# Kernel optimization log

Measured on AMD Instinct MI355X. Metric: run time of the kernel, lower is better.

The kernel has to match this reference:

```python
import jax, jax.numpy as jnp
import numpy as np

NUM_POINTS = 16384
OVERSAMPLE = 3
IMPORTANCE_RATIO = 0.75


def point_sample(feat, coords):
    """grid_sample(bilinear, align_corners=False, zero padding) at [0,1]^2 coords.
    feat: (N, C, H, W); coords: (N, P, 2) with coords[...,0]=x (width), [...,1]=y.
    Returns (N, C, P)."""
    N, C, H, W = feat.shape
    # grid_sample with g = 2c-1, align_corners=False -> pixel = c*size - 0.5
    x = coords[..., 0] * W - 0.5
    y = coords[..., 1] * H - 0.5
    x0 = jnp.floor(x)
    y0 = jnp.floor(y)
    x1 = x0 + 1.0
    y1 = y0 + 1.0
    wx1 = x - x0
    wx0 = 1.0 - wx1
    wy1 = y - y0
    wy0 = 1.0 - wy1
    featf = feat.reshape(N, C, H * W)

    def gather(yi, xi):
        valid = (xi >= 0) & (xi <= W - 1) & (yi >= 0) & (yi <= H - 1)
        xic = jnp.clip(xi, 0, W - 1).astype(jnp.int32)
        yic = jnp.clip(yi, 0, H - 1).astype(jnp.int32)
        idx = yic * W + xic  # (N, P)
        v = jnp.take_along_axis(featf, idx[:, None, :], axis=2)  # (N, C, P)
        return v * valid[:, None, :].astype(feat.dtype)

    out = (gather(y0, x0) * (wy0 * wx0)[:, None, :]
           + gather(y0, x1) * (wy0 * wx1)[:, None, :]
           + gather(y1, x0) * (wy1 * wx0)[:, None, :]
           + gather(y1, x1) * (wy1 * wx1)[:, None, :])
    return out


def calculate_uncertainty(logits):
    """logits: (N, C, P) -> (N, P) uncertainty = top2 - top1 (<= 0)."""
    if logits.shape[1] == 1:
        return -jnp.abs(logits)[:, 0, :]
    top2 = jax.lax.top_k(jnp.moveaxis(logits, 1, -1), 2)[0]  # (N, P, 2)
    return top2[..., 1] - top2[..., 0]


def sample_point_coords(coarse_logits):
    """get_uncertain_point_coords_with_randomness (torch.no_grad branch)."""
    N = coarse_logits.shape[0]
    num_sampled = NUM_POINTS * OVERSAMPLE
    num_imp = int(IMPORTANCE_RATIO * NUM_POINTS)
    num_rand = NUM_POINTS - num_imp
    k1, k2 = jax.random.split(jax.random.key(7))
    cand = jax.random.uniform(k1, (N, num_sampled, 2), dtype=jnp.float32)
    cand_logits = point_sample(coarse_logits, cand)  # (N, C, S)
    unc = calculate_uncertainty(cand_logits)  # (N, S)
    idx = jax.lax.top_k(unc, num_imp)[1]  # (N, num_imp)
    imp = jnp.take_along_axis(cand, idx[..., None], axis=1)  # (N, num_imp, 2)
    rand = jax.random.uniform(k2, (N, num_rand, 2), dtype=jnp.float32)
    return jnp.concatenate([imp, rand], axis=1)  # (N, P, 2)


def point_head(fine, coarse_pts, w0, b0, w1, b1, w2, b2, wp, bp):
    x = jnp.concatenate([fine, coarse_pts], axis=1)  # (N, nin+C, P)
    for w, b in ((w0, b0), (w1, b1), (w2, b2)):
        x = jax.nn.relu(jnp.einsum('oc,ncp->nop', w, x) + b[None, :, None])
        x = jnp.concatenate([x, coarse_pts], axis=1)  # coarse_pred_each_layer
    return jnp.einsum('oc,ncp->nop', wp, x) + bp[None, :, None]  # (N, C, P)


def setup_inputs() -> dict:
    key = jax.random.key(0)
    ks = jax.random.split(key, 8)
    N, C, Hc, Wc = 8, 19, 64, 64
    nin, Hf, Wf = 256, 128, 128
    fin = nin + C  # 275
    return {
        'coarse_sem_seg_logits': jax.random.normal(ks[0], (N, C, Hc, Wc), jnp.float32),
        'features': jax.random.normal(ks[1], (N, nin, Hf, Wf), jnp.float32),
        'w0': jax.random.normal(ks[2], (nin, fin), jnp.float32) * (2.0 / fin) ** 0.5,
        'b0': jnp.zeros((nin,), jnp.float32),
        'w1': jax.random.normal(ks[3], (nin, fin), jnp.float32) * (2.0 / fin) ** 0.5,
        'b1': jnp.zeros((nin,), jnp.float32),
        'w2': jax.random.normal(ks[4], (nin, fin), jnp.float32) * (2.0 / fin) ** 0.5,
        'b2': jnp.zeros((nin,), jnp.float32),
        'wp': jax.random.normal(ks[5], (C, fin), jnp.float32) * 0.001,
        'bp': jnp.zeros((C,), jnp.float32),
    }


def reference(coarse_sem_seg_logits, features, w0, b0, w1, b1, w2, b2, wp, bp):
    # training-mode forward of PointRendSemSegHead
    point_coords = jax.lax.stop_gradient(
        sample_point_coords(jax.lax.stop_gradient(coarse_sem_seg_logits)))
    coarse_pts = point_sample(coarse_sem_seg_logits, point_coords)  # (N, C, P)
    fine_pts = point_sample(features, point_coords)  # (N, nin, P)
    point_logits = point_head(fine_pts, coarse_pts, w0, b0, w1, b1, w2, b2, wp, bp)
    return coarse_sem_seg_logits, point_logits, point_coords
```

## Files before the change

### kernel.cpp

```cpp
#include <hip/hip_runtime.h>
#include <stdint.h>

#pragma clang fp contract(off)

#define NB    8
#define CCH   19
#define CSTR  20
#define FCH   256
#define FIN   275
#define KP    288
#define NPTS  16384
#define NSAMP 49152
#define NIMP  12288
#define NRAND 4096
#define SORT_M 65536
#define CHUNK  8192
#define TP    64
#define XROW  640
#define WBF_OFF (4u << 20)
#define CTR_OFF (4718592u)
#define FTR_OFF (8u << 20)
#define FTR_BYTES (134217728ull / 2)

typedef __attribute__((ext_vector_type(8))) short bf16x8;
typedef __attribute__((ext_vector_type(4))) float f32x4;

__host__ __device__ __forceinline__ uint32_t rotl32(uint32_t v, int r) {
  return (v << r) | (v >> (32 - r));
}

__host__ __device__ __forceinline__ void tf2x32(uint32_t k0, uint32_t k1,
                                                uint32_t x0, uint32_t x1,
                                                uint32_t* o0, uint32_t* o1) {
  const uint32_t ks2 = k0 ^ k1 ^ 0x1BD11BDAu;
  x0 += k0; x1 += k1;
#define TF_R(r) { x0 += x1; x1 = rotl32(x1, (r)); x1 ^= x0; }
  TF_R(13) TF_R(15) TF_R(26) TF_R(6)
  x0 += k1;  x1 += ks2 + 1u;
  TF_R(17) TF_R(29) TF_R(16) TF_R(24)
  x0 += ks2; x1 += k0 + 2u;
  TF_R(13) TF_R(15) TF_R(26) TF_R(6)
  x0 += k0;  x1 += k1 + 3u;
  TF_R(17) TF_R(29) TF_R(16) TF_R(24)
  x0 += k1;  x1 += ks2 + 4u;
  TF_R(13) TF_R(15) TF_R(26) TF_R(6)
  x0 += ks2; x1 += k0 + 5u;
#undef TF_R
  *o0 = x0; *o1 = x1;
}

__device__ __forceinline__ float u01_at(uint32_t k0, uint32_t k1, uint32_t i) {
  uint32_t o0, o1;
  tf2x32(k0, k1, 0u, i, &o0, &o1);
  const uint32_t b = o0 ^ o1;
  const float f = __uint_as_float((b >> 9) | 0x3f800000u) - 1.0f;
  return fmaxf(0.0f, f);
}

__device__ __forceinline__ unsigned short f2bf(float f) {
  const uint32_t u = __float_as_uint(f);
  return (unsigned short)((u + 0x7fffu + ((u >> 16) & 1u)) >> 16);
}

__device__ __forceinline__ float bf2f(unsigned short h) {
  return __uint_as_float((uint32_t)h << 16);
}

template <int SZ>
__device__ __forceinline__ void interp(float cx, float cy, int* off, float* wgt) {
  const float X = cx * (float)SZ - 0.5f, Y = cy * (float)SZ - 0.5f;
  const float x0f = floorf(X), y0f = floorf(Y);
  const float fx = X - x0f, fy = Y - y0f;
  const float wx0 = 1.0f - fx, wy0 = 1.0f - fy;
  const int x0 = (int)x0f, y0 = (int)y0f;
  const int x0c = min(max(x0, 0), SZ - 1), x1c = min(max(x0 + 1, 0), SZ - 1);
  const int y0c = min(max(y0, 0), SZ - 1), y1c = min(max(y0 + 1, 0), SZ - 1);
  const bool vx0 = (x0 >= 0) & (x0 <= SZ - 1), vx1 = (x0 >= -1) & (x0 <= SZ - 2);
  const bool vy0 = (y0 >= 0) & (y0 <= SZ - 1), vy1 = (y0 >= -1) & (y0 <= SZ - 2);
  off[0] = y0c * SZ + x0c; wgt[0] = (vy0 & vx0) ? wy0 * wx0 : 0.0f;
  off[1] = y0c * SZ + x1c; wgt[1] = (vy0 & vx1) ? wy0 * fx  : 0.0f;
  off[2] = y1c * SZ + x0c; wgt[2] = (vy1 & vx0) ? fy  * wx0 : 0.0f;
  off[3] = y1c * SZ + x1c; wgt[3] = (vy1 & vx1) ? fy  * fx  : 0.0f;
}

__global__ __launch_bounds__(256) void ctr_transpose(
    const float* __restrict__ coarse, float* __restrict__ ctr) {
  __shared__ float tile[CCH][257];
  const int b = blockIdx.x;
  const int nn = b >> 4, px0 = (b & 15) * 256;
  const int t = threadIdx.x;
  const float* src = coarse + (size_t)nn * (CCH * 4096) + px0;
#pragma unroll
  for (int c = 0; c < CCH; ++c) tile[c][t] = src[c * 4096 + t];
  __syncthreads();
  float v[CSTR];
#pragma unroll
  for (int c = 0; c < CCH; ++c) v[c] = tile[c][t];
  v[19] = 0.0f;
  float* dst = ctr + ((size_t)(nn << 12) + px0 + t) * CSTR;
#pragma unroll
  for (int k = 0; k < 5; ++k) {
    f32x4 x; x[0] = v[4*k]; x[1] = v[4*k+1]; x[2] = v[4*k+2]; x[3] = v[4*k+3];
    *(f32x4*)(dst + 4 * k) = x;
  }
}

__global__ __launch_bounds__(256) void fusedA(
    const float* __restrict__ feats, unsigned short* __restrict__ ftr,
    const float* __restrict__ ctr, unsigned long long* __restrict__ keys,
    const float* __restrict__ w0, const float* __restrict__ w1,
    const float* __restrict__ w2, const float* __restrict__ wpw,
    unsigned short* __restrict__ wbf, unsigned short* __restrict__ wpb,
    uint32_t k1a, uint32_t k1b, int use_tr) {
  __shared__ unsigned short tile[64][66];
  const int bid = blockIdx.x;
  const int t = threadIdx.x;

  if (bid < 8192) {
    if (!use_tr) return;
    const int nn = bid >> 10;
    const int ct = (bid >> 8) & 3;
    const int pt = bid & 255;
    const int c0 = ct * 64, p0 = pt * 64;
    const float* src = feats + ((size_t)nn << 22);
#pragma unroll 4
    for (int k = 0; k < 16; ++k) {
      const int c = 4 * k + (t >> 6);
      const int p = t & 63;
      tile[p][c] = f2bf(src[((size_t)(c0 + c) << 14) + p0 + p]);
    }
    __syncthreads();
    const int p = t >> 2, q = t & 3;
    const int cb = q * 16;
    uint32_t w[8];
#pragma unroll
    for (int m = 0; m < 8; ++m)
      w[m] = (uint32_t)tile[p][cb + 2 * m] | ((uint32_t)tile[p][cb + 2 * m + 1] << 16);
    unsigned short* dst = ftr + ((((size_t)nn << 14) + p0 + p) << 8) + c0 + cb;
    *(uint4*)(dst)     = make_uint4(w[0], w[1], w[2], w[3]);
    *(uint4*)(dst + 8) = make_uint4(w[4], w[5], w[6], w[7]);
  } else if (bid < 10240) {
    const int tid = (bid - 8192) * 256 + t;
    const int nn = tid >> 16, s = tid & (SORT_M - 1);
    if (s >= NSAMP) { keys[tid] = 0xFFFFFFFFFFFFFFFFull; return; }
    const uint32_t ci = (uint32_t)(((unsigned)nn * NSAMP + (unsigned)s) * 2);
    const float cx = u01_at(k1a, k1b, ci);
    const float cy = u01_at(k1a, k1b, ci + 1);
    const float X = cx * 64.0f - 0.5f, Y = cy * 64.0f - 0.5f;
    const float x0f = floorf(X), y0f = floorf(Y);
    const float fx = X - x0f, fy = Y - y0f;
    const float wx0 = 1.0f - fx, wy0 = 1.0f - fy;
    const int x0 = (int)x0f, y0 = (int)y0f;
    const int x0c = min(max(x0, 0), 63), x1c = min(max(x0 + 1, 0), 63);
    const int y0c = min(max(y0, 0), 63), y1c = min(max(y0 + 1, 0), 63);
    const bool vx0 = (x0 >= 0) & (x0 <= 63), vx1 = (x0 >= -1) & (x0 <= 62);
    const bool vy0 = (y0 >= 0) & (y0 <= 63), vy1 = (y0 >= -1) & (y0 <= 62);
    const float w00 = (vy0 & vx0) ? wy0 * wx0 : 0.0f;
    const float w01 = (vy0 & vx1) ? wy0 * fx  : 0.0f;
    const float w10 = (vy1 & vx0) ? fy  * wx0 : 0.0f;
    const float w11 = (vy1 & vx1) ? fy  * fx  : 0.0f;
    const float* rb = ctr + ((size_t)nn << 12) * CSTR;
    const float* r0 = rb + (size_t)(y0c * 64 + x0c) * CSTR;
    const float* r1 = rb + (size_t)(y0c * 64 + x1c) * CSTR;
    const float* r2 = rb + (size_t)(y1c * 64 + x0c) * CSTR;
    const float* r3 = rb + (size_t)(y1c * 64 + x1c) * CSTR;
    float m1 = -3.402823466e38f, m2 = -3.402823466e38f;
#pragma unroll
    for (int k = 0; k < 5; ++k) {
      const f32x4 x0v = *(const f32x4*)(r0 + 4 * k);
      const f32x4 x1v = *(const f32x4*)(r1 + 4 * k);
      const f32x4 x2v = *(const f32x4*)(r2 + 4 * k);
      const f32x4 x3v = *(const f32x4*)(r3 + 4 * k);
#pragma unroll
      for (int e = 0; e < 4; ++e) {
        const int c = 4 * k + e;
        if (c < CCH) {
          const float v = ((x0v[e] * w00 + x1v[e] * w01) + x2v[e] * w10) + x3v[e] * w11;
          if (v > m1) { m2 = m1; m1 = v; } else if (v > m2) { m2 = v; }
        }
      }
    }
    const float unc = m2 - m1;
    const uint32_t b = __float_as_uint(unc);
    const uint32_t asc = (b & 0x80000000u) ? ~b : (b | 0x80000000u);
    keys[tid] = ((unsigned long long)(~asc) << 32) | (uint32_t)s;
  } else {
    const int i = (bid - 10240) * 256 + t;
    if (i < 3 * 256 * KP) {
      const int L = i / (256 * KP);
      const int rem = i - L * (256 * KP);
      const int o = rem / KP, k = rem - o * KP;
      const float* W = (L == 0) ? w0 : (L == 1) ? w1 : w2;
      wbf[i] = (k < FIN) ? f2bf(W[o * FIN + k]) : (unsigned short)0;
    } else {
      const int j = i - 3 * 256 * KP;
      const int o = j / KP, k = j - o * KP;
      wpb[j] = (o < CCH && k < FIN) ? f2bf(wpw[o * FIN + k]) : (unsigned short)0;
    }
  }
}

__global__ __launch_bounds__(1024) void bitonic_local(unsigned long long* __restrict__ keys) {
  __shared__ unsigned long long s[CHUNK];
  const int cb = blockIdx.x;
  unsigned long long* a = keys + (size_t)cb * CHUNK;
  const unsigned gbase = (unsigned)(cb * CHUNK) & (SORT_M - 1);
  for (int i = threadIdx.x; i < CHUNK; i += 1024) s[i] = a[i];
  __syncthreads();
  for (int k = 2; k <= CHUNK; k <<= 1) {
    for (int j = k >> 1; j > 0; j >>= 1) {
      for (int pid = threadIdx.x; pid < CHUNK / 2; pid += 1024) {
        const int i = ((pid & ~(j - 1)) << 1) | (pid & (j - 1));
        const int l = i | j;
        const bool up = (((gbase + i) & k) == 0);
        const unsigned long long x = s[i], y = s[l];
        if ((x > y) == up) { s[i] = y; s[l] = x; }
      }
      __syncthreads();
    }
  }
  for (int i = threadIdx.x; i < CHUNK; i += 1024) a[i] = s[i];
}

__global__ __launch_bounds__(256) void bitonic_global(unsigned long long* __restrict__ keys,
                                                      int k, int j, int ppb_shift) {
  const int t = blockIdx.x * blockDim.x + threadIdx.x;
  const int b = t >> ppb_shift, pid = t & ((1 << ppb_shift) - 1);
  const int i = ((pid & ~(j - 1)) << 1) | (pid & (j - 1));
  const int l = i | j;
  const bool up = ((i & k) == 0);
  unsigned long long* a = keys + ((size_t)b << 16);
  const unsigned long long x = a[i], y = a[l];
  if ((x > y) == up) { a[i] = y; a[l] = x; }
}

__global__ __launch_bounds__(1024) void bitonic_finish(unsigned long long* __restrict__ keys,
                                                       int k) {
  __shared__ unsigned long long s[CHUNK];
  const int cb = blockIdx.x;
  unsigned long long* a = keys + (size_t)cb * CHUNK;
  const unsigned gi0 = (unsigned)(cb * CHUNK) & (SORT_M - 1);
  for (int i = threadIdx.x; i < CHUNK; i += 1024) s[i] = a[i];
  __syncthreads();
  const bool up = ((gi0 & k) == 0);
  for (int j = CHUNK >> 1; j > 0; j >>= 1) {
    for (int pid = threadIdx.x; pid < CHUNK / 2; pid += 1024) {
      const int i = ((pid & ~(j - 1)) << 1) | (pid & (j - 1));
      const int l = i | j;
      const unsigned long long x = s[i], y = s[l];
      if ((x > y) == up) { s[i] = y; s[l] = x; }
    }
    __syncthreads();
  }
  for (int i = threadIdx.x; i < CHUNK; i += 1024) a[i] = s[i];
}

__global__ __launch_bounds__(1024) void finlow_coords(
    const unsigned long long* __restrict__ keys, float* __restrict__ outc,
    uint32_t k1a, uint32_t k1b, uint32_t k2a, uint32_t k2b) {
  __shared__ unsigned long long s[CHUNK];
  const int nn = blockIdx.x >> 1, half = blockIdx.x & 1;
  const unsigned long long* a = keys + ((size_t)nn << 16) + half * CHUNK;
  for (int i = threadIdx.x; i < CHUNK; i += 1024) s[i] = a[i];
  __syncthreads();
  for (int j = CHUNK >> 1; j > 0; j >>= 1) {
    for (int pid = threadIdx.x; pid < CHUNK / 2; pid += 1024) {
      const int i = ((pid & ~(j - 1)) << 1) | (pid & (j - 1));
      const int l = i | j;
      const unsigned long long x = s[i], y = s[l];
      if (x > y) { s[i] = y; s[l] = x; }
    }
    __syncthreads();
  }
  const int pb = half * CHUNK;
  for (int q = threadIdx.x; q < CHUNK; q += 1024) {
    const int p = pb + q;
    float cx, cy;
    if (p < NIMP) {
      const unsigned idx = (unsigned)(s[q] & 0xFFFFFFFFu);
      const uint32_t ci = ((unsigned)nn * NSAMP + idx) * 2;
      cx = u01_at(k1a, k1b, ci);
      cy = u01_at(k1a, k1b, ci + 1);
    } else {
      const uint32_t ri = ((unsigned)nn * NRAND + (unsigned)(p - NIMP)) * 2;
      cx = u01_at(k2a, k2b, ri);
      cy = u01_at(k2a, k2b, ri + 1);
    }
    float* o = outc + (((size_t)nn << 14) + p) * 2;
    o[0] = cx; o[1] = cy;
  }
}

template <int USE_TR>
__global__ __launch_bounds__(512, 4) void fused_mfma(
    const float* __restrict__ coarse, const float* __restrict__ feats,
    const unsigned short* __restrict__ ftr, const float* __restrict__ ctr,
    const float* __restrict__ b0, const float* __restrict__ b1,
    const float* __restrict__ b2, const float* __restrict__ bp,
    const unsigned short* __restrict__ wbf, const unsigned short* __restrict__ wpb,
    const float* __restrict__ pc, float* __restrict__ outl) {
  __shared__ __align__(16) unsigned short xp[TP * (XROW / 2)];

  const int t = threadIdx.x;
  const int bid = ((int)blockIdx.x & 7) * 256 + ((int)blockIdx.x >> 3);
  const int nn = bid >> 8;
  const int pbase = (bid & 255) * TP;

  int offF[4]; float wgtF[4];
  int offC[4]; float wgtC[4];
  int offFc[4]; float wgtFc[4];
  {
    const float2 c = *(const float2*)(pc + ((size_t)nn * NPTS + pbase + (t >> 3)) * 2);
    interp<128>(c.x, c.y, offF, wgtF);
  }
  {
    const float2 c = *(const float2*)(pc + ((size_t)nn * NPTS + pbase + (t & 63)) * 2);
    interp<64>(c.x, c.y, offC, wgtC);
    if (!USE_TR) interp<128>(c.x, c.y, offFc, wgtFc);
  }

  if (USE_TR) {
    const int p = t >> 3, q = t & 7;
    const unsigned short* base = ftr + ((size_t)nn << 22) + q * 32;
    const unsigned short* n0 = base + ((size_t)offF[0] << 8);
    const unsigned short* n1 = base + ((size_t)offF[1] << 8);
    const unsigned short* n2 = base + ((size_t)offF[2] << 8);
    const unsigned short* n3 = base + ((size_t)offF[3] << 8);
    const float g0 = wgtF[0], g1 = wgtF[1], g2 = wgtF[2], g3 = wgtF[3];
    const unsigned swzp = (unsigned)(p & 7) << 4;
#pragma unroll
    for (int m = 0; m < 4; ++m) {
      const bf16x8 a = *(const bf16x8*)(n0 + m * 8);
      const bf16x8 bq = *(const bf16x8*)(n1 + m * 8);
      const bf16x8 c = *(const bf16x8*)(n2 + m * 8);
      const bf16x8 d = *(const bf16x8*)(n3 + m * 8);
      uint32_t u[4];
#pragma unroll
      for (int e = 0; e < 4; ++e) {
        float v0 = fmaf(bf2f((unsigned short)a[2 * e]), g0,
                   fmaf(bf2f((unsigned short)bq[2 * e]), g1,
                   fmaf(bf2f((unsigned short)c[2 * e]), g2,
                        bf2f((unsigned short)d[2 * e]) * g3)));
        float v1 = fmaf(bf2f((unsigned short)a[2 * e + 1]), g0,
                   fmaf(bf2f((unsigned short)bq[2 * e + 1]), g1,
                   fmaf(bf2f((unsigned short)c[2 * e + 1]), g2,
                        bf2f((unsigned short)d[2 * e + 1]) * g3)));
        u[e] = (uint32_t)f2bf(v0) | ((uint32_t)f2bf(v1) << 16);
      }
      *(uint4*)((char*)xp + p * XROW + (((unsigned)((q * 32 + m * 8) * 2)) ^ swzp)) =
          make_uint4(u[0], u[1], u[2], u[3]);
    }
    if (t < TP) {
      const int pp = t;
      const float* rb = ctr + ((size_t)nn << 12) * CSTR;
      const float* r0 = rb + (size_t)offC[0] * CSTR;
      const float* r1 = rb + (size_t)offC[1] * CSTR;
      const float* r2 = rb + (size_t)offC[2] * CSTR;
      const float* r3 = rb + (size_t)offC[3] * CSTR;
      const float h0 = wgtC[0], h1 = wgtC[1], h2 = wgtC[2], h3 = wgtC[3];
      unsigned short hs[32];
#pragma unroll
      for (int k = 0; k < 5; ++k) {
        const f32x4 x0v = *(const f32x4*)(r0 + 4 * k);
        const f32x4 x1v = *(const f32x4*)(r1 + 4 * k);
        const f32x4 x2v = *(const f32x4*)(r2 + 4 * k);
        const f32x4 x3v = *(const f32x4*)(r3 + 4 * k);
#pragma unroll
        for (int e = 0; e < 4; ++e) {
          const int c = 4 * k + e;
          if (c < CCH)
            hs[c] = f2bf(fmaf(x0v[e], h0, fmaf(x1v[e], h1,
                         fmaf(x2v[e], h2, x3v[e] * h3))));
        }
      }
#pragma unroll
      for (int c = CCH; c < 32; ++c) hs[c] = 0;
      const unsigned swzc = (unsigned)(pp & 7) << 4;
#pragma unroll
      for (int k = 0; k < 4; ++k) {
        uint4 u;
        u.x = (uint32_t)hs[8*k]   | ((uint32_t)hs[8*k+1] << 16);
        u.y = (uint32_t)hs[8*k+2] | ((uint32_t)hs[8*k+3] << 16);
        u.z = (uint32_t)hs[8*k+4] | ((uint32_t)hs[8*k+5] << 16);
        u.w = (uint32_t)hs[8*k+6] | ((uint32_t)hs[8*k+7] << 16);
        *(uint4*)((char*)xp + pp * XROW + (((unsigned)(512 + 16 * k)) ^ swzc)) = u;
      }
    }
  } else {
    for (int i = t; i < (KP / 2) * TP; i += 512) {
      const int p = i & (TP - 1);
      const int c0 = (i >> 6) * 2;
      float v0 = 0.0f, v1 = 0.0f;
      if (c0 < FCH) {
        const float* fb0 = feats + ((size_t)nn << 22) + ((size_t)c0 << 14);
        const float* fb1 = fb0 + 16384;
        v0 = ((fb0[offFc[0]] * wgtFc[0] + fb0[offFc[1]] * wgtFc[1])
             + fb0[offFc[2]] * wgtFc[2]) + fb0[offFc[3]] * wgtFc[3];
        v1 = ((fb1[offFc[0]] * wgtFc[0] + fb1[offFc[1]] * wgtFc[1])
             + fb1[offFc[2]] * wgtFc[2]) + fb1[offFc[3]] * wgtFc[3];
      } else if (c0 < FIN) {
        const float* cb0 = coarse + (size_t)nn * (CCH * 4096) + (size_t)(c0 - FCH) * 4096;
        v0 = ((cb0[offC[0]] * wgtC[0] + cb0[offC[1]] * wgtC[1])
             + cb0[offC[2]] * wgtC[2]) + cb0[offC[3]] * wgtC[3];
        if (c0 + 1 < FIN) {
          const float* cb1 = cb0 + 4096;
          v1 = ((cb1[offC[0]] * wgtC[0] + cb1[offC[1]] * wgtC[1])
               + cb1[offC[2]] * wgtC[2]) + cb1[offC[3]] * wgtC[3];
        }
      }
      const uint32_t u = (uint32_t)f2bf(v0) | ((uint32_t)f2bf(v1) << 16);
      *(uint32_t*)((char*)xp + p * XROW + (((unsigned)(c0 * 2)) ^ ((unsigned)(p & 7) << 4))) = u;
    }
  }

  const int lane = t & 63, wave = t >> 6;
  const int wm = wave & 3, wn = wave >> 2;
  const int l15 = lane & 15, g = lane >> 4;
  const unsigned swz = (unsigned)(l15 & 7) << 4;
  const char* xpB = (const char*)xp;

#pragma unroll
  for (int L = 0; L < 3; ++L) {
    __syncthreads();
    const float* Bv = (L == 0) ? b0 : (L == 1) ? b1 : b2;
    const unsigned short* wL = wbf + (size_t)L * (256 * KP);
    const unsigned short* wbase = wL + (size_t)(wm * 64 + l15) * KP + g * 8;

    f32x4 acc[4][2];
#pragma unroll
    for (int mt = 0; mt < 4; ++mt)
#pragma unroll
      for (int nt = 0; nt < 2; ++nt) acc[mt][nt] = (f32x4)(0.0f);

    bf16x8 a0 = *(const bf16x8*)(wbase + 0 * 16 * KP);
    bf16x8 a1 = *(const bf16x8*)(wbase + 1 * 16 * KP);
    bf16x8 a2 = *(const bf16x8*)(wbase + 2 * 16 * KP);
    bf16x8 a3 = *(const bf16x8*)(wbase + 3 * 16 * KP);
    for (int ks = 0; ks < 9; ++ks) {
      const bf16x8 c0v = a0, c1v = a1, c2v = a2, c3v = a3;
      if (ks < 8) {
        a0 = *(const bf16x8*)(wbase + 0 * 16 * KP + (ks + 1) * 32);
        a1 = *(const bf16x8*)(wbase + 1 * 16 * KP + (ks + 1) * 32);
        a2 = *(const bf16x8*)(wbase + 2 * 16 * KP + (ks + 1) * 32);
        a3 = *(const bf16x8*)(wbase + 3 * 16 * KP + (ks + 1) * 32);
      }
      const unsigned kb = (unsigned)(ks * 64 + g * 16) ^ swz;
      const bf16x8 q0 = *(const bf16x8*)(xpB + (wn * 32 + 0 + l15) * XROW + kb);
      const bf16x8 q1 = *(const bf16x8*)(xpB + (wn * 32 + 16 + l15) * XROW + kb);
      acc[0][0] = __builtin_amdgcn_mfma_f32_16x16x32_bf16(c0v, q0, acc[0][0], 0, 0, 0);
      acc[1][0] = __builtin_amdgcn_mfma_f32_16x16x32_bf16(c1v, q0, acc[1][0], 0, 0, 0);
      acc[2][0] = __builtin_amdgcn_mfma_f32_16x16x32_bf16(c2v, q0, acc[2][0], 0, 0, 0);
      acc[3][0] = __builtin_amdgcn_mfma_f32_16x16x32_bf16(c3v, q0, acc[3][0], 0, 0, 0);
      acc[0][1] = __builtin_amdgcn_mfma_f32_16x16x32_bf16(c0v, q1, acc[0][1], 0, 0, 0);
      acc[1][1] = __builtin_amdgcn_mfma_f32_16x16x32_bf16(c1v, q1, acc[1][1], 0, 0, 0);
      acc[2][1] = __builtin_amdgcn_mfma_f32_16x16x32_bf16(c2v, q1, acc[2][1], 0, 0, 0);
      acc[3][1] = __builtin_amdgcn_mfma_f32_16x16x32_bf16(c3v, q1, acc[3][1], 0, 0, 0);
    }
    __syncthreads();

#pragma unroll
    for (int mt = 0; mt < 4; ++mt) {
      const int ch0 = wm * 64 + mt * 16 + (g << 2);
      const float4 bv = *(const float4*)(Bv + ch0);
#pragma unroll
      for (int nt = 0; nt < 2; ++nt) {
        const int p = wn * 32 + nt * 16 + l15;
        const f32x4 v = acc[mt][nt];
        const unsigned short h0 = f2bf(fmaxf(v[0] + bv.x, 0.0f));
        const unsigned short h1 = f2bf(fmaxf(v[1] + bv.y, 0.0f));
        const unsigned short h2 = f2bf(fmaxf(v[2] + bv.z, 0.0f));
        const unsigned short h3 = f2bf(fmaxf(v[3] + bv.w, 0.0f));
        uint2 u;
        u.x = (uint32_t)h0 | ((uint32_t)h1 << 16);
        u.y = (uint32_t)h2 | ((uint32_t)h3 << 16);
        *(uint2*)((char*)xp + p * XROW + (((unsigned)(ch0 * 2)) ^ swz)) = u;
      }
    }
  }
  __syncthreads();

  const int hmt = wave >> 2, hnt = wave & 3;
  const unsigned short* hbase = wpb + (size_t)(hmt * 16 + l15) * KP + g * 8;
  f32x4 hacc = (f32x4)(0.0f);
  for (int ks = 0; ks < 9; ++ks) {
    const unsigned kb = (unsigned)(ks * 64 + g * 16) ^ swz;
    const bf16x8 ha = *(const bf16x8*)(hbase + ks * 32);
    const bf16x8 hb = *(const bf16x8*)(xpB + (hnt * 16 + l15) * XROW + kb);
    hacc = __builtin_amdgcn_mfma_f32_16x16x32_bf16(ha, hb, hacc, 0, 0, 0);
  }
  const int p = pbase + hnt * 16 + l15;
#pragma unroll
  for (int j = 0; j < 4; ++j) {
    const int ch = hmt * 16 + (g << 2) + j;
    if (ch < CCH)
      outl[((size_t)nn * CCH + ch) * NPTS + p] = hacc[j] + bp[ch];
  }
}

extern "C" void kernel_launch(void* const* d_in, const int* in_sizes, int n_in,
                              void* d_out, int out_size, void* d_ws, size_t ws_size,
                              hipStream_t stream) {
  const float* coarse = (const float*)d_in[0];
  const float* feats  = (const float*)d_in[1];
  const float* w0 = (const float*)d_in[2]; const float* b0 = (const float*)d_in[3];
  const float* w1 = (const float*)d_in[4]; const float* b1 = (const float*)d_in[5];
  const float* w2 = (const float*)d_in[6]; const float* b2 = (const float*)d_in[7];
  const float* wp = (const float*)d_in[8]; const float* bp = (const float*)d_in[9];

  float* out0 = (float*)d_out;
  float* outL = out0 + 622592;
  float* outC = outL + 2490368;

  unsigned long long* keys = (unsigned long long*)d_ws;
  unsigned short* wbf = (unsigned short*)((char*)d_ws + WBF_OFF);
  unsigned short* wpb = wbf + 3 * 256 * KP;
  float* ctr = (float*)((char*)d_ws + CTR_OFF);
  unsigned short* ftr = (unsigned short*)((char*)d_ws + FTR_OFF);
  const int use_tr = (ws_size >= (size_t)FTR_OFF + FTR_BYTES) ? 1 : 0;

  uint32_t k1a, k1b, k2a, k2b;
  tf2x32(0u, 7u, 0u, 0u, &k1a, &k1b);
  tf2x32(0u, 7u, 0u, 1u, &k2a, &k2b);

  hipMemcpyAsync(out0, coarse, 622592 * sizeof(float),
                 hipMemcpyDeviceToDevice, stream);

  ctr_transpose<<<128, 256, 0, stream>>>(coarse, ctr);

  fusedA<<<11140, 256, 0, stream>>>(feats, ftr, ctr, keys,
                                    w0, w1, w2, wp, wbf, wpb, k1a, k1b, use_tr);

  bitonic_local<<<64, 1024, 0, stream>>>(keys);
  bitonic_global<<<1024, 256, 0, stream>>>(keys, 16384, 8192, 15);
  bitonic_finish<<<64, 1024, 0, stream>>>(keys, 16384);
  bitonic_global<<<1024, 256, 0, stream>>>(keys, 32768, 16384, 15);
  bitonic_global<<<1024, 256, 0, stream>>>(keys, 32768, 8192, 15);
  bitonic_finish<<<64, 1024, 0, stream>>>(keys, 32768);
  bitonic_global<<<1024, 256, 0, stream>>>(keys, 65536, 32768, 15);
  bitonic_global<<<512, 256, 0, stream>>>(keys, 65536, 16384, 14);
  bitonic_global<<<256, 256, 0, stream>>>(keys, 65536, 8192, 13);
  finlow_coords<<<16, 1024, 0, stream>>>(keys, outC, k1a, k1b, k2a, k2b);

  if (use_tr)
    fused_mfma<1><<<2048, 512, 0, stream>>>(coarse, feats, ftr, ctr, b0, b1, b2,
                                            bp, wbf, wpb, outC, outL);
  else
    fused_mfma<0><<<2048, 512, 0, stream>>>(coarse, feats, ftr, ctr, b0, b1, b2,
                                            bp, wbf, wpb, outC, outL);
}
```

Baseline: 367.2 us.

## Fuse bitonic sort stages into a cooperative kernel overlapped with feature transpose

Replaces the chain of separate bitonic sort launches and the uncertainty kernel with one cooperative kernel that uses grid.sync between sort phases. Blocks 0-63 run the sort while the other 192 blocks do the feature bf16 transpose in slices spread across the phases, overlapping the two. The device-to-device memcpy and the ctr/weight prep are merged into one prep kernel. This trades many launch gaps for grid-wide barriers and limits the transpose to 192 blocks of a 256-block cooperative grid.

```diff
diff --git a/kernel.cpp b/kernel.cpp
--- a/kernel.cpp
+++ b/kernel.cpp
@@ -1,5 +1,8 @@
 #include <hip/hip_runtime.h>
+#include <hip/hip_cooperative_groups.h>
 #include <stdint.h>
+
+namespace cg = cooperative_groups;
 
 #pragma clang fp contract(off)
 
@@ -83,109 +86,62 @@
   off[3] = y1c * SZ + x1c; wgt[3] = (vy1 & vx1) ? fy  * fx  : 0.0f;
 }
 
-__global__ __launch_bounds__(256) void ctr_transpose(
-    const float* __restrict__ coarse, float* __restrict__ ctr) {
-  __shared__ float tile[CCH][257];
-  const int b = blockIdx.x;
-  const int nn = b >> 4, px0 = (b & 15) * 256;
-  const int t = threadIdx.x;
-  const float* src = coarse + (size_t)nn * (CCH * 4096) + px0;
-#pragma unroll
-  for (int c = 0; c < CCH; ++c) tile[c][t] = src[c * 4096 + t];
-  __syncthreads();
-  float v[CSTR];
-#pragma unroll
-  for (int c = 0; c < CCH; ++c) v[c] = tile[c][t];
-  v[19] = 0.0f;
-  float* dst = ctr + ((size_t)(nn << 12) + px0 + t) * CSTR;
-#pragma unroll
-  for (int k = 0; k < 5; ++k) {
-    f32x4 x; x[0] = v[4*k]; x[1] = v[4*k+1]; x[2] = v[4*k+2]; x[3] = v[4*k+3];
-    *(f32x4*)(dst + 4 * k) = x;
-  }
-}
-
-__global__ __launch_bounds__(256) void fusedA(
-    const float* __restrict__ feats, unsigned short* __restrict__ ftr,
-    const float* __restrict__ ctr, unsigned long long* __restrict__ keys,
+__device__ __forceinline__ void ftr_tile_load(const float* __restrict__ feats,
+                                              int ti, int tt,
+                                              unsigned short (*tile)[66]) {
+  const int nn = ti >> 10, ct = (ti >> 8) & 3, pt = ti & 255;
+  const int c0 = ct * 64, p0 = pt * 64;
+  const float* src = feats + ((size_t)nn << 22);
+#pragma unroll 4
+  for (int k = 0; k < 16; ++k) {
+    const int c = 4 * k + (tt >> 6);
+    const int p = tt & 63;
+    tile[p][c] = f2bf(src[((size_t)(c0 + c) << 14) + p0 + p]);
+  }
+}
+
+__device__ __forceinline__ void ftr_tile_store(unsigned short* __restrict__ ftr,
+                                               int ti, int tt,
+                                               unsigned short (*tile)[66]) {
+  const int nn = ti >> 10, ct = (ti >> 8) & 3, pt = ti & 255;
+  const int c0 = ct * 64, p0 = pt * 64;
+  const int p = tt >> 2, q = tt & 3;
+  const int cb = q * 16;
+  uint32_t w[8];
+#pragma unroll
+  for (int m = 0; m < 8; ++m)
+    w[m] = (uint32_t)tile[p][cb + 2 * m] | ((uint32_t)tile[p][cb + 2 * m + 1] << 16);
+  unsigned short* dst = ftr + ((((size_t)nn << 14) + p0 + p) << 8) + c0 + cb;
+  *(uint4*)(dst)     = make_uint4(w[0], w[1], w[2], w[3]);
+  *(uint4*)(dst + 8) = make_uint4(w[4], w[5], w[6], w[7]);
+}
+
+__global__ __launch_bounds__(256) void prep(
+    const float* __restrict__ coarse, float* __restrict__ ctr,
     const float* __restrict__ w0, const float* __restrict__ w1,
     const float* __restrict__ w2, const float* __restrict__ wpw,
     unsigned short* __restrict__ wbf, unsigned short* __restrict__ wpb,
-    uint32_t k1a, uint32_t k1b, int use_tr) {
-  __shared__ unsigned short tile[64][66];
-  const int bid = blockIdx.x;
-  const int t = threadIdx.x;
-
-  if (bid < 8192) {
-    if (!use_tr) return;
-    const int nn = bid >> 10;
-    const int ct = (bid >> 8) & 3;
-    const int pt = bid & 255;
-    const int c0 = ct * 64, p0 = pt * 64;
-    const float* src = feats + ((size_t)nn << 22);
-#pragma unroll 4
-    for (int k = 0; k < 16; ++k) {
-      const int c = 4 * k + (t >> 6);
-      const int p = t & 63;
-      tile[p][c] = f2bf(src[((size_t)(c0 + c) << 14) + p0 + p]);
-    }
+    float* __restrict__ out0) {
+  __shared__ float tile[CCH][257];
+  const int b = blockIdx.x, t = threadIdx.x;
+  if (b < 128) {
+    const int nn = b >> 4, px0 = (b & 15) * 256;
+    const float* src = coarse + (size_t)nn * (CCH * 4096) + px0;
+#pragma unroll
+    for (int c = 0; c < CCH; ++c) tile[c][t] = src[c * 4096 + t];
     __syncthreads();
-    const int p = t >> 2, q = t & 3;
-    const int cb = q * 16;
-    uint32_t w[8];
-#pragma unroll
-    for (int m = 0; m < 8; ++m)
-      w[m] = (uint32_t)tile[p][cb + 2 * m] | ((uint32_t)tile[p][cb + 2 * m + 1] << 16);
-    unsigned short* dst = ftr + ((((size_t)nn << 14) + p0 + p) << 8) + c0 + cb;
-    *(uint4*)(dst)     = make_uint4(w[0], w[1], w[2], w[3]);
-    *(uint4*)(dst + 8) = make_uint4(w[4], w[5], w[6], w[7]);
-  } else if (bid < 10240) {
-    const int tid = (bid - 8192) * 256 + t;
-    const int nn = tid >> 16, s = tid & (SORT_M - 1);
-    if (s >= NSAMP) { keys[tid] = 0xFFFFFFFFFFFFFFFFull; return; }
-    const uint32_t ci = (uint32_t)(((unsigned)nn * NSAMP + (unsigned)s) * 2);
-    const float cx = u01_at(k1a, k1b, ci);
-    const float cy = u01_at(k1a, k1b, ci + 1);
-    const float X = cx * 64.0f - 0.5f, Y = cy * 64.0f - 0.5f;
-    const float x0f = floorf(X), y0f = floorf(Y);
-    const float fx = X - x0f, fy = Y - y0f;
-    const float wx0 = 1.0f - fx, wy0 = 1.0f - fy;
-    const int x0 = (int)x0f, y0 = (int)y0f;
-    const int x0c = min(max(x0, 0), 63), x1c = min(max(x0 + 1, 0), 63);
-    const int y0c = min(max(y0, 0), 63), y1c = min(max(y0 + 1, 0), 63);
-    const bool vx0 = (x0 >= 0) & (x0 <= 63), vx1 = (x0 >= -1) & (x0 <= 62);
-    const bool vy0 = (y0 >= 0) & (y0 <= 63), vy1 = (y0 >= -1) & (y0 <= 62);
-    const float w00 = (vy0 & vx0) ? wy0 * wx0 : 0.0f;
-    const float w01 = (vy0 & vx1) ? wy0 * fx  : 0.0f;
-    const float w10 = (vy1 & vx0) ? fy  * wx0 : 0.0f;
-    const float w11 = (vy1 & vx1) ? fy  * fx  : 0.0f;
-    const float* rb = ctr + ((size_t)nn << 12) * CSTR;
-    const float* r0 = rb + (size_t)(y0c * 64 + x0c) * CSTR;
-    const float* r1 = rb + (size_t)(y0c * 64 + x1c) * CSTR;
-    const float* r2 = rb + (size_t)(y1c * 64 + x0c) * CSTR;
-    const float* r3 = rb + (size_t)(y1c * 64 + x1c) * CSTR;
-    float m1 = -3.402823466e38f, m2 = -3.402823466e38f;
+    float v[CSTR];
+#pragma unroll
+    for (int c = 0; c < CCH; ++c) v[c] = tile[c][t];
+    v[19] = 0.0f;
+    float* dst = ctr + ((size_t)(nn << 12) + px0 + t) * CSTR;
 #pragma unroll
     for (int k = 0; k < 5; ++k) {
-      const f32x4 x0v = *(const f32x4*)(r0 + 4 * k);
-      const f32x4 x1v = *(const f32x4*)(r1 + 4 * k);
-      const f32x4 x2v = *(const f32x4*)(r2 + 4 * k);
-      const f32x4 x3v = *(const f32x4*)(r3 + 4 * k);
-#pragma unroll
-      for (int e = 0; e < 4; ++e) {
-        const int c = 4 * k + e;
-        if (c < CCH) {
-          const float v = ((x0v[e] * w00 + x1v[e] * w01) + x2v[e] * w10) + x3v[e] * w11;
-          if (v > m1) { m2 = m1; m1 = v; } else if (v > m2) { m2 = v; }
-        }
-      }
-    }
-    const float unc = m2 - m1;
-    const uint32_t b = __float_as_uint(unc);
-    const uint32_t asc = (b & 0x80000000u) ? ~b : (b | 0x80000000u);
-    keys[tid] = ((unsigned long long)(~asc) << 32) | (uint32_t)s;
-  } else {
-    const int i = (bid - 10240) * 256 + t;
+      f32x4 x; x[0] = v[4*k]; x[1] = v[4*k+1]; x[2] = v[4*k+2]; x[3] = v[4*k+3];
+      *(f32x4*)(dst + 4 * k) = x;
+    }
+  } else if (b < 1028) {
+    const int i = (b - 128) * 256 + t;
     if (i < 3 * 256 * KP) {
       const int L = i / (256 * KP);
       const int rem = i - L * (256 * KP);
@@ -197,97 +153,185 @@
       const int o = j / KP, k = j - o * KP;
       wpb[j] = (o < CCH && k < FIN) ? f2bf(wpw[o * FIN + k]) : (unsigned short)0;
     }
-  }
-}
-
-__global__ __launch_bounds__(1024) void bitonic_local(unsigned long long* __restrict__ keys) {
-  __shared__ unsigned long long s[CHUNK];
-  const int cb = blockIdx.x;
-  unsigned long long* a = keys + (size_t)cb * CHUNK;
-  const unsigned gbase = (unsigned)(cb * CHUNK) & (SORT_M - 1);
-  for (int i = threadIdx.x; i < CHUNK; i += 1024) s[i] = a[i];
-  __syncthreads();
-  for (int k = 2; k <= CHUNK; k <<= 1) {
-    for (int j = k >> 1; j > 0; j >>= 1) {
-      for (int pid = threadIdx.x; pid < CHUNK / 2; pid += 1024) {
-        const int i = ((pid & ~(j - 1)) << 1) | (pid & (j - 1));
-        const int l = i | j;
-        const bool up = (((gbase + i) & k) == 0);
-        const unsigned long long x = s[i], y = s[l];
-        if ((x > y) == up) { s[i] = y; s[l] = x; }
-      }
-      __syncthreads();
-    }
-  }
-  for (int i = threadIdx.x; i < CHUNK; i += 1024) a[i] = s[i];
-}
-
-__global__ __launch_bounds__(256) void bitonic_global(unsigned long long* __restrict__ keys,
-                                                      int k, int j, int ppb_shift) {
-  const int t = blockIdx.x * blockDim.x + threadIdx.x;
-  const int b = t >> ppb_shift, pid = t & ((1 << ppb_shift) - 1);
+  } else {
+    const int i4 = (b - 1028) * 256 + t;
+    ((float4*)out0)[i4] = ((const float4*)coarse)[i4];
+  }
+}
+
+__device__ __forceinline__ void unc_slot(const float* __restrict__ ctr,
+                                         unsigned long long* __restrict__ keys,
+                                         uint32_t k1a, uint32_t k1b, int tid) {
+  const int nn = tid >> 16, sIdx = tid & (SORT_M - 1);
+  if (sIdx >= NSAMP) { keys[tid] = 0xFFFFFFFFFFFFFFFFull; return; }
+  const uint32_t ci = (uint32_t)(((unsigned)nn * NSAMP + (unsigned)sIdx) * 2);
+  const float cx = u01_at(k1a, k1b, ci);
+  const float cy = u01_at(k1a, k1b, ci + 1);
+  const float X = cx * 64.0f - 0.5f, Y = cy * 64.0f - 0.5f;
+  const float x0f = floorf(X), y0f = floorf(Y);
+  const float fx = X - x0f, fy = Y - y0f;
+  const float wx0 = 1.0f - fx, wy0 = 1.0f - fy;
+  const int x0 = (int)x0f, y0 = (int)y0f;
+  const int x0c = min(max(x0, 0), 63), x1c = min(max(x0 + 1, 0), 63);
+  const int y0c = min(max(y0, 0), 63), y1c = min(max(y0 + 1, 0), 63);
+  const bool vx0 = (x0 >= 0) & (x0 <= 63), vx1 = (x0 >= -1) & (x0 <= 62);
+  const bool vy0 = (y0 >= 0) & (y0 <= 63), vy1 = (y0 >= -1) & (y0 <= 62);
+  const float w00 = (vy0 & vx0) ? wy0 * wx0 : 0.0f;
+  const float w01 = (vy0 & vx1) ? wy0 * fx  : 0.0f;
+  const float w10 = (vy1 & vx0) ? fy  * wx0 : 0.0f;
+  const float w11 = (vy1 & vx1) ? fy  * fx  : 0.0f;
+  const float* rb = ctr + ((size_t)nn << 12) * CSTR;
+  const float* r0 = rb + (size_t)(y0c * 64 + x0c) * CSTR;
+  const float* r1 = rb + (size_t)(y0c * 64 + x1c) * CSTR;
+  const float* r2 = rb + (size_t)(y1c * 64 + x0c) * CSTR;
+  const float* r3 = rb + (size_t)(y1c * 64 + x1c) * CSTR;
+  float m1 = -3.402823466e38f, m2 = -3.402823466e38f;
+#pragma unroll
+  for (int k = 0; k < 5; ++k) {
+    const f32x4 x0v = *(const f32x4*)(r0 + 4 * k);
+    const f32x4 x1v = *(const f32x4*)(r1 + 4 * k);
+    const f32x4 x2v = *(const f32x4*)(r2 + 4 * k);
+    const f32x4 x3v = *(const f32x4*)(r3 + 4 * k);
+#pragma unroll
+    for (int e = 0; e < 4; ++e) {
+      const int c = 4 * k + e;
+      if (c < CCH) {
+        const float v = ((x0v[e] * w00 + x1v[e] * w01) + x2v[e] * w10) + x3v[e] * w11;
+        if (v > m1) { m2 = m1; m1 = v; } else if (v > m2) { m2 = v; }
+      }
+    }
+  }
+  const float unc = m2 - m1;
+  const uint32_t b = __float_as_uint(unc);
+  const uint32_t asc = (b & 0x80000000u) ? ~b : (b | 0x80000000u);
+  keys[tid] = ((unsigned long long)(~asc) << 32) | (uint32_t)sIdx;
+}
+
+__device__ __forceinline__ void cx_step(unsigned long long* __restrict__ keys,
+                                        int k, int j, int shift, int idx) {
+  const int bb = idx >> shift, pid = idx & ((1 << shift) - 1);
   const int i = ((pid & ~(j - 1)) << 1) | (pid & (j - 1));
   const int l = i | j;
   const bool up = ((i & k) == 0);
-  unsigned long long* a = keys + ((size_t)b << 16);
+  unsigned long long* a = keys + ((size_t)bb << 16);
   const unsigned long long x = a[i], y = a[l];
   if ((x > y) == up) { a[i] = y; a[l] = x; }
 }
 
-__global__ __launch_bounds__(1024) void bitonic_finish(unsigned long long* __restrict__ keys,
-                                                       int k) {
-  __shared__ unsigned long long s[CHUNK];
-  const int cb = blockIdx.x;
-  unsigned long long* a = keys + (size_t)cb * CHUNK;
-  const unsigned gi0 = (unsigned)(cb * CHUNK) & (SORT_M - 1);
-  for (int i = threadIdx.x; i < CHUNK; i += 1024) s[i] = a[i];
-  __syncthreads();
-  const bool up = ((gi0 & k) == 0);
-  for (int j = CHUNK >> 1; j > 0; j >>= 1) {
-    for (int pid = threadIdx.x; pid < CHUNK / 2; pid += 1024) {
-      const int i = ((pid & ~(j - 1)) << 1) | (pid & (j - 1));
-      const int l = i | j;
-      const unsigned long long x = s[i], y = s[l];
-      if ((x > y) == up) { s[i] = y; s[l] = x; }
-    }
-    __syncthreads();
-  }
-  for (int i = threadIdx.x; i < CHUNK; i += 1024) a[i] = s[i];
-}
-
-__global__ __launch_bounds__(1024) void finlow_coords(
-    const unsigned long long* __restrict__ keys, float* __restrict__ outc,
-    uint32_t k1a, uint32_t k1b, uint32_t k2a, uint32_t k2b) {
-  __shared__ unsigned long long s[CHUNK];
-  const int nn = blockIdx.x >> 1, half = blockIdx.x & 1;
-  const unsigned long long* a = keys + ((size_t)nn << 16) + half * CHUNK;
-  for (int i = threadIdx.x; i < CHUNK; i += 1024) s[i] = a[i];
-  __syncthreads();
-  for (int j = CHUNK >> 1; j > 0; j >>= 1) {
-    for (int pid = threadIdx.x; pid < CHUNK / 2; pid += 1024) {
-      const int i = ((pid & ~(j - 1)) << 1) | (pid & (j - 1));
-      const int l = i | j;
-      const unsigned long long x = s[i], y = s[l];
-      if (x > y) { s[i] = y; s[l] = x; }
-    }
-    __syncthreads();
-  }
-  const int pb = half * CHUNK;
-  for (int q = threadIdx.x; q < CHUNK; q += 1024) {
-    const int p = pb + q;
-    float cx, cy;
-    if (p < NIMP) {
-      const unsigned idx = (unsigned)(s[q] & 0xFFFFFFFFu);
-      const uint32_t ci = ((unsigned)nn * NSAMP + idx) * 2;
-      cx = u01_at(k1a, k1b, ci);
-      cy = u01_at(k1a, k1b, ci + 1);
-    } else {
-      const uint32_t ri = ((unsigned)nn * NRAND + (unsigned)(p - NIMP)) * 2;
-      cx = u01_at(k2a, k2b, ri);
-      cy = u01_at(k2a, k2b, ri + 1);
-    }
-    float* o = outc + (((size_t)nn << 14) + p) * 2;
-    o[0] = cx; o[1] = cy;
+__global__ __launch_bounds__(1024) void coop_pipe(
+    const float* __restrict__ ctr, unsigned long long* __restrict__ keys,
+    const float* __restrict__ feats, unsigned short* __restrict__ ftr,
+    float* __restrict__ outc,
+    uint32_t k1a, uint32_t k1b, uint32_t k2a, uint32_t k2b, int use_tr) {
+  __shared__ unsigned long long sbuf[CHUNK];
+  const int b = blockIdx.x, t = threadIdx.x;
+  cg::grid_group grid = cg::this_grid();
+
+  {
+    const int gid = b * 1024 + t;
+    unc_slot(ctr, keys, k1a, k1b, gid * 2);
+    unc_slot(ctr, keys, k1a, k1b, gid * 2 + 1);
+  }
+  grid.sync();
+
+  for (int p = 1; p <= 10; ++p) {
+    if (b < 64) {
+      unsigned long long* a = keys + (size_t)b * CHUNK;
+      const unsigned gbase = (unsigned)(b * CHUNK) & (SORT_M - 1);
+      if (p == 1) {
+        for (int i = t; i < CHUNK; i += 1024) sbuf[i] = a[i];
+        __syncthreads();
+        for (int k = 2; k <= CHUNK; k <<= 1) {
+          for (int j = k >> 1; j > 0; j >>= 1) {
+            for (int pid = t; pid < CHUNK / 2; pid += 1024) {
+              const int i = ((pid & ~(j - 1)) << 1) | (pid & (j - 1));
+              const int l = i | j;
+              const bool up = (((gbase + i) & k) == 0);
+              const unsigned long long x = sbuf[i], y = sbuf[l];
+              if ((x > y) == up) { sbuf[i] = y; sbuf[l] = x; }
+            }
+            __syncthreads();
+          }
+        }
+        for (int i = t; i < CHUNK; i += 1024) a[i] = sbuf[i];
+      } else if (p == 3 || p == 6) {
+        const int k = (p == 3) ? 16384 : 32768;
+        for (int i = t; i < CHUNK; i += 1024) sbuf[i] = a[i];
+        __syncthreads();
+        const bool up = ((gbase & k) == 0);
+        for (int j = CHUNK >> 1; j > 0; j >>= 1) {
+          for (int pid = t; pid < CHUNK / 2; pid += 1024) {
+            const int i = ((pid & ~(j - 1)) << 1) | (pid & (j - 1));
+            const int l = i | j;
+            const unsigned long long x = sbuf[i], y = sbuf[l];
+            if ((x > y) == up) { sbuf[i] = y; sbuf[l] = x; }
+          }
+          __syncthreads();
+        }
+        for (int i = t; i < CHUNK; i += 1024) a[i] = sbuf[i];
+      } else if (p == 2 || p == 4 || p == 5 || p == 7) {
+        int k, j;
+        if (p == 2)      { k = 16384; j = 8192;  }
+        else if (p == 4) { k = 32768; j = 16384; }
+        else if (p == 5) { k = 32768; j = 8192;  }
+        else             { k = 65536; j = 32768; }
+        const int base = b * 1024 + t;
+#pragma unroll
+        for (int w = 0; w < 4; ++w)
+          cx_step(keys, k, j, 15, base + (w << 16));
+      } else if (p == 8) {
+        const int base = b * 1024 + t;
+        cx_step(keys, 65536, 16384, 14, base);
+        cx_step(keys, 65536, 16384, 14, base + 65536);
+      } else if (p == 9) {
+        cx_step(keys, 65536, 8192, 13, b * 1024 + t);
+      } else {
+        if (b < 16) {
+          const int nn = b >> 1, half = b & 1;
+          const unsigned long long* src = keys + ((size_t)nn << 16) + half * CHUNK;
+          for (int i = t; i < CHUNK; i += 1024) sbuf[i] = src[i];
+          __syncthreads();
+          for (int j = CHUNK >> 1; j > 0; j >>= 1) {
+            for (int pid = t; pid < CHUNK / 2; pid += 1024) {
+              const int i = ((pid & ~(j - 1)) << 1) | (pid & (j - 1));
+              const int l = i | j;
+              const unsigned long long x = sbuf[i], y = sbuf[l];
+              if (x > y) { sbuf[i] = y; sbuf[l] = x; }
+            }
+            __syncthreads();
+          }
+          const int pb = half * CHUNK;
+          for (int q = t; q < CHUNK; q += 1024) {
+            const int pp = pb + q;
+            float cx, cy;
+            if (pp < NIMP) {
+              const unsigned idx = (unsigned)(sbuf[q] & 0xFFFFFFFFu);
+              const uint32_t ci = ((unsigned)nn * NSAMP + idx) * 2;
+              cx = u01_at(k1a, k1b, ci);
+              cy = u01_at(k1a, k1b, ci + 1);
+            } else {
+              const uint32_t ri = ((unsigned)nn * NRAND + (unsigned)(pp - NIMP)) * 2;
+              cx = u01_at(k2a, k2b, ri);
+              cy = u01_at(k2a, k2b, ri + 1);
+            }
+            float* o = outc + (((size_t)nn << 14) + pp) * 2;
+            o[0] = cx; o[1] = cy;
+          }
+        }
+      }
+    } else if (use_tr) {
+      for (int j = (p - 1) * 11 / 10; j < p * 11 / 10; ++j) {
+        const int q = (b - 64) + 192 * j;
+        const int ti = q * 4 + (t >> 8);
+        unsigned short (*tp)[66] =
+            (unsigned short (*)[66])((char*)sbuf + (size_t)(t >> 8) * (64 * 66 * 2));
+        if (ti < 8192) ftr_tile_load(feats, ti, t & 255, tp);
+        __syncthreads();
+        if (ti < 8192) ftr_tile_store(ftr, ti, t & 255, tp);
+        __syncthreads();
+      }
+    }
+    if (p < 10) grid.sync();
   }
 }
 
@@ -516,30 +560,21 @@
   unsigned short* wpb = wbf + 3 * 256 * KP;
   float* ctr = (float*)((char*)d_ws + CTR_OFF);
   unsigned short* ftr = (unsigned short*)((char*)d_ws + FTR_OFF);
-  const int use_tr = (ws_size >= (size_t)FTR_OFF + FTR_BYTES) ? 1 : 0;
+  int use_tr = (ws_size >= (size_t)FTR_OFF + FTR_BYTES) ? 1 : 0;
 
   uint32_t k1a, k1b, k2a, k2b;
   tf2x32(0u, 7u, 0u, 0u, &k1a, &k1b);
   tf2x32(0u, 7u, 0u, 1u, &k2a, &k2b);
 
-  hipMemcpyAsync(out0, coarse, 622592 * sizeof(float),
-                 hipMemcpyDeviceToDevice, stream);
-
-  ctr_transpose<<<128, 256, 0, stream>>>(coarse, ctr);
-
-  fusedA<<<11140, 256, 0, stream>>>(feats, ftr, ctr, keys,
-                                    w0, w1, w2, wp, wbf, wpb, k1a, k1b, use_tr);
-
-  bitonic_local<<<64, 1024, 0, stream>>>(keys);
-  bitonic_global<<<1024, 256, 0, stream>>>(keys, 16384, 8192, 15);
-  bitonic_finish<<<64, 1024, 0, stream>>>(keys, 16384);
-  bitonic_global<<<1024, 256, 0, stream>>>(keys, 32768, 16384, 15);
-  bitonic_global<<<1024, 256, 0, stream>>>(keys, 32768, 8192, 15);
-  bitonic_finish<<<64, 1024, 0, stream>>>(keys, 32768);
-  bitonic_global<<<1024, 256, 0, stream>>>(keys, 65536, 32768, 15);
-  bitonic_global<<<512, 256, 0, stream>>>(keys, 65536, 16384, 14);
-  bitonic_global<<<256, 256, 0, stream>>>(keys, 65536, 8192, 13);
-  finlow_coords<<<16, 1024, 0, stream>>>(keys, outC, k1a, k1b, k2a, k2b);
+  prep<<<1636, 256, 0, stream>>>(coarse, ctr, w0, w1, w2, wp, wbf, wpb, out0);
+
+  const float* ctr_c = ctr;
+  const float* feats_c = feats;
+  void* cargs[] = {(void*)&ctr_c, (void*)&keys, (void*)&feats_c, (void*)&ftr,
+                   (void*)&outC, (void*)&k1a, (void*)&k1b, (void*)&k2a,
+                   (void*)&k2b, (void*)&use_tr};
+  hipLaunchCooperativeKernel((void*)coop_pipe, dim3(256), dim3(1024),
+                             cargs, 0, stream);
 
   if (use_tr)
     fused_mfma<1><<<2048, 512, 0, stream>>>(coarse, feats, ftr, ctr, b0, b1, b2,
```

New measurement: 668.6 us (median of 2 runs). 82.1% more time.
